# Optimization experiments

Measured on AMD Instinct MI355X. Metric: run time of the kernel, lower is better.

## Reference

```python
import jax, jax.numpy as jnp
import numpy as np

N_ATOMS = 16384
APC = 64            # atoms per conformer
N_CONF = 256        # 64 mols * 4 confs
N_MOL = 64
DEG = 32
E = N_ATOMS * DEG
H = 128             # hidden_channels = num_filters = out_channels
G = 50              # num_gaussians
L = 6               # num_interactions
CUTOFF = 10.0
LOG2 = float(np.log(2.0))


def ssp(x):
    # ShiftedSoftplus: softplus(x) - log(2)
    return jax.nn.softplus(x) - LOG2


def setup_inputs() -> dict:
    key = jax.random.key(0)
    ks = jax.random.split(key, 24)
    rng = np.random.default_rng(0)

    z = jnp.asarray(rng.integers(1, 100, size=(N_ATOMS,)), dtype=jnp.int64 if jax.config.jax_enable_x64 else jnp.int32)
    # positions uniform in a 5A box -> all intra-conformer distances < cutoff
    pos = jax.random.uniform(ks[0], (N_ATOMS, 3), dtype=jnp.float32) * 5.0

    # within-conformer random edges, no self loops (radius_graph surrogate)
    i = np.repeat(np.arange(N_ATOMS), DEG)
    off = rng.integers(1, APC, size=E)
    j = (i // APC) * APC + (i % APC + off) % APC
    edge_index = jnp.asarray(np.stack([j, i]), dtype=jnp.int32)  # [2,E] (source, target)

    atom_to_conf = jnp.asarray(np.arange(N_ATOMS) // APC, dtype=jnp.int32)
    conf_to_mol = jnp.asarray(np.arange(N_CONF) // (N_CONF // N_MOL), dtype=jnp.int32)

    s = 0.05
    p = {
        'emb':     jax.random.normal(ks[1], (120, H), jnp.float32) * s,
        # per-interaction stacked params [L, ...]
        'mlp_w1':  jax.random.normal(ks[2], (L, G, H), jnp.float32) * s,
        'mlp_b1':  jnp.zeros((L, H), jnp.float32),
        'mlp_w2':  jax.random.normal(ks[3], (L, H, H), jnp.float32) * s,
        'mlp_b2':  jnp.zeros((L, H), jnp.float32),
        'cf_w1':   jax.random.normal(ks[4], (L, H, H), jnp.float32) * s,
        'cf_w2':   jax.random.normal(ks[5], (L, H, H), jnp.float32) * s,
        'cf_b2':   jnp.zeros((L, H), jnp.float32),
        'int_w':   jax.random.normal(ks[6], (L, H, H), jnp.float32) * s,
        'int_b':   jnp.zeros((L, H), jnp.float32),
        # readout head
        'out_w1':  jax.random.normal(ks[7], (H, H), jnp.float32) * s,
        'out_b1':  jnp.zeros((H,), jnp.float32),
        'out_w2':  jax.random.normal(ks[8], (H, H), jnp.float32) * s,
        'out_b2':  jnp.zeros((H,), jnp.float32),
        'head_w1': jax.random.normal(ks[9], (H, H // 2), jnp.float32) * s,
        'head_b1': jnp.zeros((H // 2,), jnp.float32),
        'head_w2': jax.random.normal(ks[10], (H // 2, 1), jnp.float32) * s,
        'head_b2': jnp.zeros((1,), jnp.float32),
    }
    return dict(z=z, pos=pos, edge_index=edge_index, atom_to_conf=atom_to_conf,
                conf_to_mol=conf_to_mol, **p)


def reference(z, pos, edge_index, atom_to_conf, conf_to_mol, emb,
              mlp_w1, mlp_b1, mlp_w2, mlp_b2, cf_w1, cf_w2, cf_b2,
              int_w, int_b, out_w1, out_b1, out_w2, out_b2,
              head_w1, head_b1, head_w2, head_b2):
    row, col = edge_index[0], edge_index[1]  # message from row, aggregated at col

    h = emb[z]                                             # [N,H]
    edge_weight = jnp.linalg.norm(pos[row] - pos[col], axis=-1)  # [E]

    # GaussianSmearing
    offset = jnp.linspace(0.0, CUTOFF, G)
    coeff = -0.5 / (offset[1] - offset[0]) ** 2
    edge_attr = jnp.exp(coeff * (edge_weight[:, None] - offset[None, :]) ** 2)  # [E,G]

    C = 0.5 * (jnp.cos(edge_weight * jnp.pi / CUTOFF) + 1.0)  # cosine cutoff [E]

    for l in range(L):
        # filter network on edge features, modulated by cutoff envelope
        Wf = ssp(edge_attr @ mlp_w1[l] + mlp_b1[l]) @ mlp_w2[l] + mlp_b2[l]
        Wf = Wf * C[:, None]                               # [E,H]
        xf = h @ cf_w1[l]                                  # lin1 (no bias) [N,H]
        msg = xf[row] * Wf                                 # gather * filter [E,H]
        agg = jax.ops.segment_sum(msg, col, num_segments=N_ATOMS)  # scatter-add [N,H]
        xc = agg @ cf_w2[l] + cf_b2[l]                     # lin2
        h = h + (ssp(xc) @ int_w[l] + int_b[l])            # act, lin, residual

    h = ssp(h @ out_w1 + out_b1)
    h = h @ out_w2 + out_b2                                # [N,H]

    conf_emb = jax.ops.segment_sum(h, atom_to_conf, num_segments=N_CONF)   # [C,H]
    mol_emb = jax.ops.segment_sum(conf_emb, conf_to_mol, num_segments=N_MOL)  # [M,H]

    out = (ssp(mol_emb @ head_w1 + head_b1) @ head_w2 + head_b2)[:, 0]  # [M]
    return out
```

## Files before the change

### kernel.cpp

```cpp
#include <hip/hip_runtime.h>
#include <math.h>

#define N_ATOMS 16384
#define APC 64
#define N_CONF 256
#define N_MOL 64
#define DEG 32
#define NEDGE (N_ATOMS * DEG)
#define H 128
#define G 50
#define NL 6
#define TP0 512
#define TPB 4096
#define CUTOFF 10.0f

typedef __attribute__((ext_vector_type(8))) short short8_t;
typedef __attribute__((ext_vector_type(8))) _Float16 half8_t;
typedef __attribute__((ext_vector_type(4))) float f32x4;
typedef __attribute__((ext_vector_type(2))) float f32x2;

__device__ __forceinline__ float ssp_f(float x) {
  float e = __expf(-fabsf(x));
  return fmaxf(x, 0.f) + __logf(1.f + e) - 0.69314718055994531f;
}
__device__ __forceinline__ unsigned short bf16_rne(float x) {
  unsigned u = __float_as_uint(x);
  unsigned r = u + 0x7FFF + ((u >> 16) & 1);
  return (unsigned short)(r >> 16);
}
__device__ __forceinline__ float bf16_to_f(unsigned short s) {
  return __uint_as_float(((unsigned)s) << 16);
}
__device__ __forceinline__ float bflo(unsigned u) { return __uint_as_float(u << 16); }
__device__ __forceinline__ float bfhi(unsigned u) { return __uint_as_float(u & 0xFFFF0000u); }

__device__ __forceinline__ uint2 pack4h(const f32x4 v) {
  union { _Float16 h[4]; uint2 u; } x;
  x.h[0] = (_Float16)v[0];
  x.h[1] = (_Float16)v[1];
  x.h[2] = (_Float16)v[2];
  x.h[3] = (_Float16)v[3];
  return x.u;
}
__device__ __forceinline__ void unpack4h(uint2 u, float* o) {
  union { uint2 u; _Float16 h[4]; } x;
  x.u = u;
  o[0] = (float)x.h[0];
  o[1] = (float)x.h[1];
  o[2] = (float)x.h[2];
  o[3] = (float)x.h[3];
}

__global__ __launch_bounds__(256) void k_setup(
    const float* __restrict__ pos, const int* __restrict__ esrc,
    const int* __restrict__ etgt, int* __restrict__ pk,
    const float* __restrict__ cf_w1, const float* __restrict__ cf_w2,
    const float* __restrict__ int_w, const float* __restrict__ out_w1,
    const float* __restrict__ out_w2, _Float16* __restrict__ PW,
    const float* __restrict__ w1, const float* __restrict__ b1,
    const float* __restrict__ w2, const float* __restrict__ b2,
    float* __restrict__ T, int* __restrict__ cnt) {
  __shared__ float g2[2][64];
  __shared__ float S2[2][128];
  const int b = blockIdx.x;
  const int tid = threadIdx.x;
  if (b == 0 && tid == 0) *cnt = 0;
  if (b < 2048) {
    int e = b * 256 + tid;
    int r = esrc[e], c = etgt[e];
    float dx = pos[r * 3 + 0] - pos[c * 3 + 0];
    float dy = pos[r * 3 + 1] - pos[c * 3 + 1];
    float dz = pos[r * 3 + 2] - pos[c * 3 + 2];
    float d = sqrtf(dx * dx + dy * dy + dz * dz);
    int i = (int)(d * ((float)(TPB - 1) / CUTOFF) + 0.5f);
    if (i > TPB - 1) i = TPB - 1;
    if (i < 0) i = 0;
    pk[e] = (i << 8) | ((r & (APC - 1)) << 20);
  } else if (b < 2208) {
    int e = (b - 2048) * 256 + tid;
    int g = e >> 11, t = e & 2047;
    int kb = t >> 9, rem = t & 511, nt = rem >> 6, lane = rem & 63;
    int quad = lane >> 4, ln = lane & 15;
    int kbase = kb * 32 + quad * 8;
    int n = nt * 16 + ln;
    const float* src;
    if (g < 12) {
      int l = g >> 1;
      src = (g & 1) ? (int_w + l * 16384) : (cf_w2 + l * 16384);
    } else if (g < 18) {
      src = cf_w1 + (g - 12) * 16384;
    } else {
      src = (g == 18) ? out_w1 : out_w2;
    }
    half8_t hv;
    #pragma unroll
    for (int j = 0; j < 8; j++) hv[j] = (_Float16)src[(kbase + j) * H + n];
    *(half8_t*)&PW[(size_t)g * 16384 + (size_t)t * 8] = hv;
  } else {
    int bb = b - 2208;
    const int l = bb >> 8;
    const int grp = tid >> 7;
    const int c = tid & 127;
    const int p = (bb & 255) * 2 + grp;
    const float d = (float)p * (CUTOFF / (float)(TP0 - 1));
    const float gspace = CUTOFF / (float)(G - 1);
    const float coeff = -0.5f / (gspace * gspace);
    if (c < G) {
      float x = d - (float)c * gspace;
      g2[grp][c] = __expf(coeff * x * x);
    }
    __syncthreads();
    const float* W1 = w1 + l * G * H;
    float s = b1[l * H + c];
    #pragma unroll 5
    for (int i = 0; i < G; i++) s += g2[grp][i] * W1[i * H + c];
    S2[grp][c] = ssp_f(s);
    __syncthreads();
    const float* W2 = w2 + l * H * H;
    float o = b2[l * H + c];
    #pragma unroll 8
    for (int j = 0; j < H; j++) o += S2[grp][j] * W2[j * H + c];
    float Cc = 0.5f * (__cosf(d * (3.14159265358979f / CUTOFF)) + 1.f);
    T[((size_t)l * TP0 + p) * H + c] = o * Cc;
  }
}

__global__ __launch_bounds__(256) void k_up(const float* __restrict__ T,
                                            unsigned short* __restrict__ Tb) {
  int t = blockIdx.x * 256 + threadIdx.x;
  int l = t >> 17;
  int rem = t & 131071;
  int p4 = rem >> 5, cg = rem & 31;
  int c = cg * 4;
  float u = (float)p4 * ((float)(TP0 - 1) / (float)(TPB - 1));
  int i = (int)u;
  if (i > TP0 - 2) i = TP0 - 2;
  float f = u - (float)i;
  const float* a = T + ((size_t)l * TP0 + i) * H + c;
  float4 v0 = *(const float4*)a;
  float4 v1 = *(const float4*)(a + H);
  ushort4 o;
  o.x = bf16_rne(v0.x + f * (v1.x - v0.x));
  o.y = bf16_rne(v0.y + f * (v1.y - v0.y));
  o.z = bf16_rne(v0.z + f * (v1.z - v0.z));
  o.w = bf16_rne(v0.w + f * (v1.w - v0.w));
  int dst = (cg < 16) ? cg * 8 : (cg - 16) * 8 + 4;
  *(ushort4*)&Tb[((size_t)l * TPB + p4) * H + dst] = o;
}

#define MFMA16(a, b, c) __builtin_amdgcn_mfma_f32_16x16x32_f16((a), (b), (c), 0, 0, 0)

struct BF {
  half8_t h[4];
};
__device__ __forceinline__ BF load_B(const _Float16* __restrict__ pw, int nt, int lane) {
  BF b;
  #pragma unroll
  for (int kb = 0; kb < 4; kb++)
    b.h[kb] = *(const half8_t*)(pw + ((size_t)(kb * 8 + nt) * 64 + lane) * 8);
  return b;
}

__device__ __forceinline__ void gemm_rt2(const _Float16 (*A)[136],
                                         const BF& b, int rt2, int quad, int ln,
                                         f32x4 acc[2]) {
  #pragma unroll
  for (int kb = 0; kb < 4; kb++) {
    int ko = kb * 32 + quad * 8;
    #pragma unroll
    for (int rtt = 0; rtt < 2; rtt++) {
      int row = rt2 * 32 + rtt * 16 + ln;
      half8_t ah = *(const half8_t*)&A[row][ko];
      acc[rtt] = MFMA16(ah, b.h[kb], acc[rtt]);
    }
  }
}

__device__ __forceinline__ void gemm_rt2T(const _Float16 (*A)[136],
                                          const BF& b, int rt2, int quad, int ln,
                                          f32x4 acc[2]) {
  #pragma unroll
  for (int kb = 0; kb < 4; kb++) {
    int ko = kb * 32 + quad * 8;
    #pragma unroll
    for (int rtt = 0; rtt < 2; rtt++) {
      int row = rt2 * 32 + rtt * 16 + ln;
      half8_t ah = *(const half8_t*)&A[row][ko];
      acc[rtt] = MFMA16(b.h[kb], ah, acc[rtt]);
    }
  }
}

#define AGG_BODY(A2, MSARR, TVARR)                                             \
  {                                                                            \
    f32x2 ac0 = {0.f, 0.f}, ac1 = {0.f, 0.f}, ac2 = {0.f, 0.f},                \
          ac3 = {0.f, 0.f};                                                    \
    _Pragma("unroll") for (int it = 0; it < 8; it++) {                         \
      int sl = MSARR[it] >> 20;                                                \
      const float* xr = &xs[sl][c0];                                           \
      float4 x0 = *(const float4*)xr;                                          \
      float4 x1 = *(const float4*)(xr + 64);                                   \
      uint4 tv = TVARR[it];                                                    \
      ac0 = __builtin_elementwise_fma((f32x2){bflo(tv.x), bfhi(tv.x)},         \
                                      (f32x2){x0.x, x0.y}, ac0);               \
      ac1 = __builtin_elementwise_fma((f32x2){bflo(tv.y), bfhi(tv.y)},         \
                                      (f32x2){x0.z, x0.w}, ac1);               \
      ac2 = __builtin_elementwise_fma((f32x2){bflo(tv.z), bfhi(tv.z)},         \
                                      (f32x2){x1.x, x1.y}, ac2);               \
      ac3 = __builtin_elementwise_fma((f32x2){bflo(tv.w), bfhi(tv.w)},         \
                                      (f32x2){x1.z, x1.w}, ac3);               \
    }                                                                          \
    float accs[8] = {ac0.x, ac0.y, ac1.x, ac1.y, ac2.x, ac2.y, ac3.x, ac3.y};  \
    _Pragma("unroll") for (int j = 0; j < 8; j++) {                            \
      accs[j] += __shfl_xor(accs[j], 16);                                      \
      accs[j] += __shfl_xor(accs[j], 32);                                      \
    }                                                                          \
    float va =                                                                 \
        eg == 0 ? accs[0] : eg == 1 ? accs[2] : eg == 2 ? accs[4] : accs[6];   \
    float vb =                                                                 \
        eg == 0 ? accs[1] : eg == 1 ? accs[3] : eg == 2 ? accs[5] : accs[7];   \
    union { _Float16 h[2]; short2 s; } uu;                                     \
    uu.h[0] = (_Float16)va;                                                    \
    uu.h[1] = (_Float16)vb;                                                    \
    int cw = (eg >> 1) * 64 + c0 + (eg & 1) * 2;                               \
    *(short2*)&S1[A2][cw] = uu.s;                                              \
  }

__global__ __launch_bounds__(1024, 1) void k_mega(
    const int* __restrict__ z, const float* __restrict__ emb,
    const int* __restrict__ pk, const unsigned short* __restrict__ Tb,
    const _Float16* __restrict__ PW, const float* __restrict__ cf_b2,
    const float* __restrict__ int_b, const float* __restrict__ out_b1,
    const float* __restrict__ out_b2, float* __restrict__ ce,
    const float* __restrict__ hw1, const float* __restrict__ hb1,
    const float* __restrict__ hw2, const float* __restrict__ hb2,
    int* __restrict__ cnt, float* __restrict__ outp) {
  __shared__ float xs[64][128];
  __shared__ __align__(16) _Float16 hs[64][136];
  __shared__ __align__(16) _Float16 ts[64][136];
  __shared__ __align__(16) _Float16 S1[64][136];
  __shared__ int pks[2048];
  __shared__ float ps[2][128];
  __shared__ int is_last;
  const int conf = blockIdx.x;
  const int tid = threadIdx.x;
  const int lane = tid & 63, w = tid >> 6;
  const int quad = lane >> 4, ln = lane & 15;
  const int rt2 = w & 1, nt = w >> 1;
  const int eg = lane >> 4, c0 = (lane & 15) * 4;
  const int colb = nt * 16 + quad * 4;

  pks[tid] = pk[conf * 2048 + tid];
  pks[tid + 1024] = pk[conf * 2048 + 1024 + tid];

  {
    int r = tid >> 4, cb = (tid & 15) * 8;
    const float* src = emb + (size_t)z[conf * 64 + r] * H + cb;
    float4 v0 = *(const float4*)src, v1 = *(const float4*)(src + 4);
    half8_t hv;
    hv[0] = (_Float16)v0.x; hv[1] = (_Float16)v0.y;
    hv[2] = (_Float16)v0.z; hv[3] = (_Float16)v0.w;
    hv[4] = (_Float16)v1.x; hv[5] = (_Float16)v1.y;
    hv[6] = (_Float16)v1.z; hv[7] = (_Float16)v1.w;
    *(half8_t*)&hs[r][cb] = hv;
  }
  BF bX = load_B(PW + (size_t)12 * 16384, nt, lane);
  __syncthreads();

  int msP[8];
  uint4 tvP[8];

  {
    f32x4 acc[2] = {{0.f, 0.f, 0.f, 0.f}, {0.f, 0.f, 0.f, 0.f}};
    gemm_rt2T(hs, bX, rt2, quad, ln, acc);
    #pragma unroll
    for (int rtt = 0; rtt < 2; rtt++)
      *(f32x4*)&xs[rt2 * 32 + rtt * 16 + ln][colb] = acc[rtt];
  }
  {
    const char* T0 = (const char*)Tb + ln * 16;
    #pragma unroll
    for (int it = 0; it < 8; it++) {
      msP[it] = pks[(w * 4) * DEG + it * 4 + eg];
      tvP[it] = *(const uint4*)(T0 + (msP[it] & 0xFFFFF));
    }
  }
  __syncthreads();

  BF bN;

  for (int l = 0; l < NL; l++) {
    const char* Tlb = (const char*)(Tb + (size_t)l * TPB * H) + ln * 16;
    AGG_BODY(w * 4, msP, tvP)
    #pragma unroll 1
    for (int aa = 1; aa < 4; aa++) {
      int a2 = w * 4 + aa;
      int ms[8];
      uint4 tvv[8];
      #pragma unroll
      for (int it = 0; it < 8; it++) {
        ms[it] = pks[a2 * DEG + it * 4 + eg];
        tvv[it] = *(const uint4*)(Tlb + (ms[it] & 0xFFFFF));
      }
      AGG_BODY(a2, ms, tvv)
    }
    bN = load_B(PW + (size_t)(2 * l) * 16384, nt, lane);
    __syncthreads();
    {
      f32x4 acc[2] = {{0.f, 0.f, 0.f, 0.f}, {0.f, 0.f, 0.f, 0.f}};
      gemm_rt2T(S1, bN, rt2, quad, ln, acc);
      f32x4 bb4 = *(const f32x4*)&cf_b2[l * H + colb];
      #pragma unroll
      for (int rtt = 0; rtt < 2; rtt++) {
        int row = rt2 * 32 + rtt * 16 + ln;
        f32x4 v;
        #pragma unroll
        for (int reg = 0; reg < 4; reg++) v[reg] = ssp_f(acc[rtt][reg] + bb4[reg]);
        *(uint2*)&ts[row][colb] = pack4h(v);
      }
    }
    bN = load_B(PW + (size_t)(2 * l + 1) * 16384, nt, lane);
    __syncthreads();
    {
      f32x4 acc[2] = {{0.f, 0.f, 0.f, 0.f}, {0.f, 0.f, 0.f, 0.f}};
      gemm_rt2T(ts, bN, rt2, quad, ln, acc);
      f32x4 bb4 = *(const f32x4*)&int_b[l * H + colb];
      #pragma unroll
      for (int rtt = 0; rtt < 2; rtt++) {
        int row = rt2 * 32 + rtt * 16 + ln;
        float hv[4];
        unpack4h(*(const uint2*)&hs[row][colb], hv);
        f32x4 v;
        #pragma unroll
        for (int reg = 0; reg < 4; reg++)
          v[reg] = acc[rtt][reg] + bb4[reg] + hv[reg];
        *(uint2*)&hs[row][colb] = pack4h(v);
      }
    }
    bN = load_B(PW + (size_t)((l < NL - 1) ? (13 + l) : 18) * 16384, nt, lane);
    __syncthreads();
    if (l < NL - 1) {
      f32x4 acc[2] = {{0.f, 0.f, 0.f, 0.f}, {0.f, 0.f, 0.f, 0.f}};
      gemm_rt2T(hs, bN, rt2, quad, ln, acc);
      #pragma unroll
      for (int rtt = 0; rtt < 2; rtt++)
        *(f32x4*)&xs[rt2 * 32 + rtt * 16 + ln][colb] = acc[rtt];
      const char* Tn = (const char*)(Tb + (size_t)(l + 1) * TPB * H) + ln * 16;
      #pragma unroll
      for (int it = 0; it < 8; it++) {
        msP[it] = pks[(w * 4) * DEG + it * 4 + eg];
        tvP[it] = *(const uint4*)(Tn + (msP[it] & 0xFFFFF));
      }
      __syncthreads();
    }
  }

  {
    f32x4 acc[2] = {{0.f, 0.f, 0.f, 0.f}, {0.f, 0.f, 0.f, 0.f}};
    gemm_rt2T(hs, bN, rt2, quad, ln, acc);
    f32x4 bb4 = *(const f32x4*)&out_b1[colb];
    #pragma unroll
    for (int rtt = 0; rtt < 2; rtt++) {
      int row = rt2 * 32 + rtt * 16 + ln;
      f32x4 v;
      #pragma unroll
      for (int reg = 0; reg < 4; reg++) v[reg] = ssp_f(acc[rtt][reg] + bb4[reg]);
      *(uint2*)&ts[row][colb] = pack4h(v);
    }
  }
  bN = load_B(PW + (size_t)19 * 16384, nt, lane);
  __syncthreads();
  {
    f32x4 acc[2] = {{0.f, 0.f, 0.f, 0.f}, {0.f, 0.f, 0.f, 0.f}};
    gemm_rt2(ts, bN, rt2, quad, ln, acc);
    int col = nt * 16 + ln;
    float s = acc[0][0] + acc[0][1] + acc[0][2] + acc[0][3] +
              acc[1][0] + acc[1][1] + acc[1][2] + acc[1][3];
    s += __shfl_xor(s, 16);
    s += __shfl_xor(s, 32);
    if (quad == 0) ps[rt2][col] = s;
  }
  __syncthreads();
  if (tid < 128) {
    float v = ps[0][tid] + ps[1][tid] + 64.f * out_b2[tid];
    __hip_atomic_store(&ce[conf * 128 + tid], v, __ATOMIC_RELAXED,
                       __HIP_MEMORY_SCOPE_AGENT);
  }
  __syncthreads();
  if (tid == 0) {
    __threadfence();
    int old = __hip_atomic_fetch_add(cnt, 1, __ATOMIC_ACQ_REL,
                                     __HIP_MEMORY_SCOPE_AGENT);
    is_last = (old == N_CONF - 1) ? 1 : 0;
  }
  __syncthreads();
  if (is_last) {
    __threadfence();
    float* mol = &xs[0][0];
    for (int t = tid; t < N_MOL * 128; t += 1024) {
      int m = t >> 7, c = t & 127;
      const float* b = ce + (size_t)(m * 4) * 128;
      float s = __hip_atomic_load(&b[c], __ATOMIC_RELAXED, __HIP_MEMORY_SCOPE_AGENT) +
                __hip_atomic_load(&b[128 + c], __ATOMIC_RELAXED, __HIP_MEMORY_SCOPE_AGENT) +
                __hip_atomic_load(&b[256 + c], __ATOMIC_RELAXED, __HIP_MEMORY_SCOPE_AGENT) +
                __hip_atomic_load(&b[384 + c], __ATOMIC_RELAXED, __HIP_MEMORY_SCOPE_AGENT);
      mol[t] = s;
    }
    __syncthreads();
    float* q = (float*)&S1[0][0];
    for (int t = tid; t < N_MOL * 64; t += 1024) {
      int m = t >> 6, j = t & 63;
      float qq = hb1[j];
      #pragma unroll 8
      for (int c = 0; c < H; c++) qq += mol[m * 128 + c] * hw1[c * 64 + j];
      q[t] = ssp_f(qq);
    }
    __syncthreads();
    if (tid < N_MOL) {
      float o = hb2[0];
      #pragma unroll 8
      for (int j = 0; j < 64; j++) o += q[tid * 64 + j] * hw2[j];
      outp[tid] = o;
    }
  }
}

extern "C" void kernel_launch(void* const* d_in, const int* in_sizes, int n_in,
                              void* d_out, int out_size, void* d_ws, size_t ws_size,
                              hipStream_t stream) {
  const int*   z       = (const int*)d_in[0];
  const float* pos     = (const float*)d_in[1];
  const int*   eidx    = (const int*)d_in[2];
  const float* emb     = (const float*)d_in[5];
  const float* mlp_w1  = (const float*)d_in[6];
  const float* mlp_b1  = (const float*)d_in[7];
  const float* mlp_w2  = (const float*)d_in[8];
  const float* mlp_b2  = (const float*)d_in[9];
  const float* cf_w1   = (const float*)d_in[10];
  const float* cf_w2   = (const float*)d_in[11];
  const float* cf_b2   = (const float*)d_in[12];
  const float* int_w   = (const float*)d_in[13];
  const float* int_b   = (const float*)d_in[14];
  const float* out_w1  = (const float*)d_in[15];
  const float* out_b1  = (const float*)d_in[16];
  const float* out_w2  = (const float*)d_in[17];
  const float* out_b2  = (const float*)d_in[18];
  const float* head_w1 = (const float*)d_in[19];
  const float* head_b1 = (const float*)d_in[20];
  const float* head_w2 = (const float*)d_in[21];
  const float* head_b2 = (const float*)d_in[22];

  char* ws = (char*)d_ws;
  float*          T   = (float*)ws;
  unsigned short* Tb  = (unsigned short*)(ws + (size_t)NL * TP0 * H * 4);
  char*           p2  = (char*)Tb + (size_t)NL * TPB * H * 2;
  int*            pk  = (int*)p2;
  _Float16*       PW  = (_Float16*)(p2 + (size_t)NEDGE * 4);
  float*          ce  = (float*)((char*)PW + (size_t)20 * 16384 * 2);
  int*            cnt = (int*)((char*)ce + (size_t)N_CONF * H * 4);

  k_setup<<<3744, 256, 0, stream>>>(pos, eidx, eidx + NEDGE, pk,
                                    cf_w1, cf_w2, int_w, out_w1, out_w2, PW,
                                    mlp_w1, mlp_b1, mlp_w2, mlp_b2, T, cnt);
  k_up<<<(NL * TPB * H / 4) / 256, 256, 0, stream>>>(T, Tb);

  k_mega<<<N_CONF, 1024, 0, stream>>>(z, emb, pk, Tb, PW, cf_b2, int_b,
                                      out_b1, out_b2, ce,
                                      head_w1, head_b1, head_w2, head_b2,
                                      cnt, (float*)d_out);
}
```

Measured before the change: 215.8 us.

## Fuse filter-table upsampling into setup kernel and keep residual in registers

Removes the separate k_up launch. Each filter-table block of the setup kernel now computes the few coarse points it needs into shared memory, then linearly interpolates and writes its 16 fine bf16 rows directly, so the fp32 intermediate table is no longer written and reread. The extra cost is that neighbouring blocks recompute overlapping coarse points, four per block instead of two. Separately, the megakernel keeps the residual hidden state in fp32 registers across interactions rather than unpacking it from fp16 shared memory each layer, which removes LDS reads and may slightly change numerics.

Result: slower. 224.5 us (+4.0%).

```diff
diff --git a/kernel.cpp b/kernel.cpp
--- a/kernel.cpp
+++ b/kernel.cpp
@@ -28,9 +28,6 @@
   unsigned r = u + 0x7FFF + ((u >> 16) & 1);
   return (unsigned short)(r >> 16);
 }
-__device__ __forceinline__ float bf16_to_f(unsigned short s) {
-  return __uint_as_float(((unsigned)s) << 16);
-}
 __device__ __forceinline__ float bflo(unsigned u) { return __uint_as_float(u << 16); }
 __device__ __forceinline__ float bfhi(unsigned u) { return __uint_as_float(u & 0xFFFF0000u); }
 
@@ -59,9 +56,10 @@
     const float* __restrict__ out_w2, _Float16* __restrict__ PW,
     const float* __restrict__ w1, const float* __restrict__ b1,
     const float* __restrict__ w2, const float* __restrict__ b2,
-    float* __restrict__ T, int* __restrict__ cnt) {
-  __shared__ float g2[2][64];
+    unsigned short* __restrict__ Tb, int* __restrict__ cnt) {
+  __shared__ float g2s[2][64];
   __shared__ float S2[2][128];
+  __shared__ float OutS[4][132];
   const int b = blockIdx.x;
   const int tid = threadIdx.x;
   if (b == 0 && tid == 0) *cnt = 0;
@@ -98,54 +96,54 @@
     *(half8_t*)&PW[(size_t)g * 16384 + (size_t)t * 8] = hv;
   } else {
     int bb = b - 2208;
-    const int l = bb >> 8;
-    const int grp = tid >> 7;
-    const int c = tid & 127;
-    const int p = (bb & 255) * 2 + grp;
-    const float d = (float)p * (CUTOFF / (float)(TP0 - 1));
+    const int l = bb >> 8, q = bb & 255;
+    const int grp = tid >> 7, c = tid & 127;
+    const int p_min =
+        (int)((float)(q * 16) * ((float)(TP0 - 1) / (float)(TPB - 1)));
     const float gspace = CUTOFF / (float)(G - 1);
     const float coeff = -0.5f / (gspace * gspace);
-    if (c < G) {
-      float x = d - (float)c * gspace;
-      g2[grp][c] = __expf(coeff * x * x);
-    }
-    __syncthreads();
     const float* W1 = w1 + l * G * H;
-    float s = b1[l * H + c];
-    #pragma unroll 5
-    for (int i = 0; i < G; i++) s += g2[grp][i] * W1[i * H + c];
-    S2[grp][c] = ssp_f(s);
-    __syncthreads();
     const float* W2 = w2 + l * H * H;
-    float o = b2[l * H + c];
-    #pragma unroll 8
-    for (int j = 0; j < H; j++) o += S2[grp][j] * W2[j * H + c];
-    float Cc = 0.5f * (__cosf(d * (3.14159265358979f / CUTOFF)) + 1.f);
-    T[((size_t)l * TP0 + p) * H + c] = o * Cc;
-  }
-}
-
-__global__ __launch_bounds__(256) void k_up(const float* __restrict__ T,
-                                            unsigned short* __restrict__ Tb) {
-  int t = blockIdx.x * 256 + threadIdx.x;
-  int l = t >> 17;
-  int rem = t & 131071;
-  int p4 = rem >> 5, cg = rem & 31;
-  int c = cg * 4;
-  float u = (float)p4 * ((float)(TP0 - 1) / (float)(TPB - 1));
-  int i = (int)u;
-  if (i > TP0 - 2) i = TP0 - 2;
-  float f = u - (float)i;
-  const float* a = T + ((size_t)l * TP0 + i) * H + c;
-  float4 v0 = *(const float4*)a;
-  float4 v1 = *(const float4*)(a + H);
-  ushort4 o;
-  o.x = bf16_rne(v0.x + f * (v1.x - v0.x));
-  o.y = bf16_rne(v0.y + f * (v1.y - v0.y));
-  o.z = bf16_rne(v0.z + f * (v1.z - v0.z));
-  o.w = bf16_rne(v0.w + f * (v1.w - v0.w));
-  int dst = (cg < 16) ? cg * 8 : (cg - 16) * 8 + 4;
-  *(ushort4*)&Tb[((size_t)l * TPB + p4) * H + dst] = o;
+    #pragma unroll 1
+    for (int r = 0; r < 2; r++) {
+      int pt = r * 2 + grp;
+      int p = p_min + pt;
+      if (p > TP0 - 1) p = TP0 - 1;
+      float d = (float)p * (CUTOFF / (float)(TP0 - 1));
+      if (c < G) {
+        float x = d - (float)c * gspace;
+        g2s[grp][c] = __expf(coeff * x * x);
+      }
+      __syncthreads();
+      float s = b1[l * H + c];
+      #pragma unroll 5
+      for (int i = 0; i < G; i++) s += g2s[grp][i] * W1[i * H + c];
+      S2[grp][c] = ssp_f(s);
+      __syncthreads();
+      float o = b2[l * H + c];
+      #pragma unroll 8
+      for (int j = 0; j < H; j++) o += S2[grp][j] * W2[j * H + c];
+      float Cc = 0.5f * (__cosf(d * (3.14159265358979f / CUTOFF)) + 1.f);
+      OutS[pt][c] = o * Cc;
+      __syncthreads();
+    }
+    int p4o = tid >> 4, cg = tid & 15;
+    int p4 = q * 16 + p4o;
+    float u = (float)p4 * ((float)(TP0 - 1) / (float)(TPB - 1));
+    int i = (int)u;
+    if (i > TP0 - 2) i = TP0 - 2;
+    float f = u - (float)i;
+    int li = i - p_min;
+    short8_t ov;
+    #pragma unroll
+    for (int j = 0; j < 4; j++) {
+      float a0 = OutS[li][cg * 4 + j], a1 = OutS[li + 1][cg * 4 + j];
+      ov[j] = (short)bf16_rne(a0 + f * (a1 - a0));
+      float b0 = OutS[li][64 + cg * 4 + j], b1v = OutS[li + 1][64 + cg * 4 + j];
+      ov[4 + j] = (short)bf16_rne(b0 + f * (b1v - b0));
+    }
+    *(short8_t*)&Tb[((size_t)l * TPB + p4) * H + cg * 8] = ov;
+  }
 }
 
 #define MFMA16(a, b, c) __builtin_amdgcn_mfma_f32_16x16x32_f16((a), (b), (c), 0, 0, 0)
@@ -270,6 +268,16 @@
   int msP[8];
   uint4 tvP[8];
 
+  f32x4 hreg[2];
+  #pragma unroll
+  for (int rtt = 0; rtt < 2; rtt++) {
+    int row = rt2 * 32 + rtt * 16 + ln;
+    float hv[4];
+    unpack4h(*(const uint2*)&hs[row][colb], hv);
+    hreg[rtt][0] = hv[0]; hreg[rtt][1] = hv[1];
+    hreg[rtt][2] = hv[2]; hreg[rtt][3] = hv[3];
+  }
+
   {
     f32x4 acc[2] = {{0.f, 0.f, 0.f, 0.f}, {0.f, 0.f, 0.f, 0.f}};
     gemm_rt2T(hs, bX, rt2, quad, ln, acc);
@@ -328,12 +336,11 @@
       #pragma unroll
       for (int rtt = 0; rtt < 2; rtt++) {
         int row = rt2 * 32 + rtt * 16 + ln;
-        float hv[4];
-        unpack4h(*(const uint2*)&hs[row][colb], hv);
         f32x4 v;
         #pragma unroll
         for (int reg = 0; reg < 4; reg++)
-          v[reg] = acc[rtt][reg] + bb4[reg] + hv[reg];
+          v[reg] = acc[rtt][reg] + bb4[reg] + hreg[rtt][reg];
+        hreg[rtt] = v;
         *(uint2*)&hs[row][colb] = pack4h(v);
       }
     }
@@ -451,8 +458,7 @@
   const float* head_b2 = (const float*)d_in[22];
 
   char* ws = (char*)d_ws;
-  float*          T   = (float*)ws;
-  unsigned short* Tb  = (unsigned short*)(ws + (size_t)NL * TP0 * H * 4);
+  unsigned short* Tb  = (unsigned short*)ws;
   char*           p2  = (char*)Tb + (size_t)NL * TPB * H * 2;
   int*            pk  = (int*)p2;
   _Float16*       PW  = (_Float16*)(p2 + (size_t)NEDGE * 4);
@@ -461,8 +467,7 @@
 
   k_setup<<<3744, 256, 0, stream>>>(pos, eidx, eidx + NEDGE, pk,
                                     cf_w1, cf_w2, int_w, out_w1, out_w2, PW,
-                                    mlp_w1, mlp_b1, mlp_w2, mlp_b2, T, cnt);
-  k_up<<<(NL * TPB * H / 4) / 256, 256, 0, stream>>>(T, Tb);
+                                    mlp_w1, mlp_b1, mlp_w2, mlp_b2, Tb, cnt);
 
   k_mega<<<N_CONF, 1024, 0, stream>>>(z, emb, pk, Tb, PW, cf_b2, int_b,
                                       out_b1, out_b2, ce,
```
